# Performance work log

Measured on AMD Instinct MI355X. Metric: run time of the kernel, lower is better.

The kernel has to match this reference:

```python
import jax, jax.numpy as jnp
import numpy as np

N_NODES = 50000


def gcn_conv(x, W, b, src, dst, num_nodes):
    """PyG GCNConv: add self-loops, symmetric deg^{-1/2} normalization,
    linear transform, scatter-add aggregation, bias."""
    loop = jnp.arange(num_nodes, dtype=src.dtype)
    s = jnp.concatenate([src, loop])  # message sources
    d = jnp.concatenate([dst, loop])  # message destinations
    deg = jax.ops.segment_sum(jnp.ones_like(d, dtype=x.dtype), d, num_segments=num_nodes)
    dinv = jnp.where(deg > 0, jax.lax.rsqrt(deg), 0.0)
    norm = dinv[s] * dinv[d]                      # [E+N]
    h = x @ W                                      # [N, out]
    msg = h[s] * norm[:, None]                     # gather + scale  [E+N, out]
    out = jax.ops.segment_sum(msg, d, num_segments=num_nodes)  # scatter-add
    return out + b


def setup_inputs() -> dict:
    key = jax.random.key(0)
    ks = jax.random.split(key, 8)
    n, e = N_NODES, 1600000
    d_in, d_h, d_out = 128, 128, 64
    x = jax.random.normal(ks[0], (n, d_in), dtype=jnp.float32)
    edge_index = jax.random.randint(ks[1], (2, e), 0, n, dtype=jnp.int32)
    s = 1.0 / np.sqrt(d_in)
    W1 = jax.random.uniform(ks[2], (d_in, d_h), jnp.float32, -s, s)
    b1 = jnp.zeros((d_h,), jnp.float32)
    W2 = jax.random.uniform(ks[3], (d_h, d_h), jnp.float32, -s, s)
    b2 = jnp.zeros((d_h,), jnp.float32)
    W3 = jax.random.uniform(ks[4], (d_h, d_out), jnp.float32, -s, s)
    b3 = jnp.zeros((d_out,), jnp.float32)
    return {"x": x, "edge_index": edge_index, "W1": W1, "b1": b1,
            "W2": W2, "b2": b2, "W3": W3, "b3": b3}


def reference(x, edge_index, W1, b1, W2, b2, W3, b3):
    src, dst = edge_index[0], edge_index[1]
    n = x.shape[0]
    # Dropout in eval mode (identity); ReLU between GCN layers.
    h = jax.nn.relu(gcn_conv(x, W1, b1, src, dst, n))
    h = jax.nn.relu(gcn_conv(h, W2, b2, src, dst, n))
    out = gcn_conv(h, W3, b3, src, dst, n)
    return out
```

## Files before the change

kernel.cpp:

```cpp
#include <hip/hip_runtime.h>
#include <type_traits>


#define EPB  4096
#define DIRW 197

typedef __attribute__((ext_vector_type(8))) short bf16x8;
typedef __attribute__((ext_vector_type(4))) float f32x4;
typedef __attribute__((ext_vector_type(2))) float f32x2;

__device__ __forceinline__ unsigned short f2bf(float f) {
    unsigned int u = __float_as_uint(f);
    u += 0x7FFFu + ((u >> 16) & 1u);
    return (unsigned short)(u >> 16);
}
__device__ __forceinline__ float bflo(unsigned int u) { return __uint_as_float(u << 16); }
__device__ __forceinline__ float bfhi(unsigned int u) { return __uint_as_float(u & 0xFFFF0000u); }

__global__ __launch_bounds__(256) void bin_kernel(const int* __restrict__ src,
                                                  const int* __restrict__ dst,
                                                  unsigned int* __restrict__ pair_buf,
                                                  int* __restrict__ dir,
                                                  int E, int nbkt) {
    __shared__ unsigned int stage[EPB];
    __shared__ int hist[DIRW];
    __shared__ int sc[256];
    __shared__ int cur[DIRW];
    int tid = threadIdx.x;
    int blk = blockIdx.x;
    if (tid < DIRW) hist[tid] = 0;
    __syncthreads();

    int s_reg[16], d_reg[16];
#pragma unroll
    for (int j = 0; j < 16; ++j) {
        int gi = blk * EPB + j * 256 + tid;
        int s = 0, d = nbkt << 8;
        if (gi < E) { s = src[gi]; d = dst[gi]; }
        s_reg[j] = s; d_reg[j] = d;
        atomicAdd(&hist[d >> 8], 1);
    }
    __syncthreads();
    int h = (tid < DIRW) ? hist[tid] : 0;
    sc[tid] = h;
    __syncthreads();
#pragma unroll
    for (int off = 1; off < 256; off <<= 1) {
        int v = (tid >= off) ? sc[tid - off] : 0;
        __syncthreads();
        sc[tid] += v;
        __syncthreads();
    }
    if (tid < DIRW) {
        int st = sc[tid] - h;
        cur[tid] = st;
        dir[blk * DIRW + tid] = st;
    }
    __syncthreads();
#pragma unroll
    for (int j = 0; j < 16; ++j) {
        int b = d_reg[j] >> 8;
        int slot = atomicAdd(&cur[b], 1);
        stage[slot] = ((unsigned int)s_reg[j] << 8) | (unsigned int)(d_reg[j] & 255);
    }
    __syncthreads();
#pragma unroll
    for (int j = 0; j < 16; ++j) {
        int idx = j * 256 + tid;
        pair_buf[blk * EPB + idx] = stage[idx];
    }
}

__global__ __launch_bounds__(512) void csr_sizes_kernel(const unsigned int* __restrict__ pair_buf,
                                                        const int* __restrict__ dir,
                                                        int* __restrict__ bucket_pad,
                                                        int* __restrict__ node_cnt,
                                                        float* __restrict__ dinv,
                                                        int NB, int n) {
    __shared__ int dstart[400];
    __shared__ int dend[400];
    __shared__ int cnt[256];
    int tid = threadIdx.x;
    int b = blockIdx.x;
    for (int i = tid; i < NB; i += 512) {
        dstart[i] = dir[i * DIRW + b];
        dend[i]   = dir[i * DIRW + b + 1];
    }
    if (tid < 256) cnt[tid] = 0;
    __syncthreads();
    int wid = tid >> 6, lane = tid & 63;
    for (int seg = wid; seg < NB; seg += 8) {
        int s0 = dstart[seg], s1 = dend[seg];
        for (int k = s0 + lane; k < s1; k += 64) {
            unsigned int p = pair_buf[(size_t)seg * EPB + k];
            atomicAdd(&cnt[p & 255u], 1);
        }
    }
    __syncthreads();
    if (tid < 256) {
        node_cnt[b * 256 + tid] = cnt[tid];
        int d = b * 256 + tid;
        if (d < n) dinv[d] = rsqrtf((float)(cnt[tid] + 1));
    }
    if (tid < 64) {
        int m = max(max(cnt[4 * tid], cnt[4 * tid + 1]),
                    max(cnt[4 * tid + 2], cnt[4 * tid + 3]));
        int L = (m + 7) & ~7;
        int s = L;
#pragma unroll
        for (int off = 1; off < 64; off <<= 1) s += __shfl_xor(s, off);
        if (tid == 0) bucket_pad[b] = 4 * s;
    }
}

__global__ __launch_bounds__(256) void bucket_scan_kernel(const int* __restrict__ bucket_pad,
                                                          int* __restrict__ bucket_base,
                                                          int* __restrict__ row_ptr,
                                                          unsigned int* __restrict__ hb_pad_row,
                                                          int nbkt, int n) {
    __shared__ int sc[256];
    int tid = threadIdx.x;
    if (tid < 32) hb_pad_row[tid] = 0u;
    int h = (tid < nbkt) ? bucket_pad[tid] : 0;
    sc[tid] = h;
    __syncthreads();
#pragma unroll
    for (int off = 1; off < 256; off <<= 1) {
        int v = (tid >= off) ? sc[tid - off] : 0;
        __syncthreads();
        sc[tid] += v;
        __syncthreads();
    }
    if (tid <= nbkt) bucket_base[tid] = sc[tid] - h;
    if (tid == nbkt) row_ptr[n] = sc[tid] - h;
}

__global__ __launch_bounds__(512) void csr_place_kernel(const unsigned int* __restrict__ pair_buf,
                                                        const int* __restrict__ dir,
                                                        const int* __restrict__ bucket_base,
                                                        const int* __restrict__ node_cnt,
                                                        int* __restrict__ row_ptr,
                                                        int* __restrict__ csr_src,
                                                        int n, int NB) {
    __shared__ int dstart[400];
    __shared__ int dend[400];
    __shared__ int Lg[64];
    __shared__ int Lpre[64];
    __shared__ int nbase[256];
    __shared__ int cur[256];
    __shared__ int cend[256];
    int tid = threadIdx.x;
    int b = blockIdx.x;
    for (int i = tid; i < NB; i += 512) {
        dstart[i] = dir[i * DIRW + b];
        dend[i]   = dir[i * DIRW + b + 1];
    }
    __syncthreads();
    if (tid < 64) {
        int c0 = node_cnt[b * 256 + 4 * tid + 0];
        int c1 = node_cnt[b * 256 + 4 * tid + 1];
        int c2 = node_cnt[b * 256 + 4 * tid + 2];
        int c3 = node_cnt[b * 256 + 4 * tid + 3];
        int m = max(max(c0, c1), max(c2, c3));
        int L = (m + 7) & ~7;
        int x = L;
#pragma unroll
        for (int off = 1; off < 64; off <<= 1) {
            int y = __shfl_up(x, off);
            if (tid >= off) x += y;
        }
        Lg[tid] = L;
        Lpre[tid] = x - L;
    }
    __syncthreads();
    int base = bucket_base[b];
    if (tid < 256) {
        int g = tid >> 2;
        int nb = base + 4 * Lpre[g] + (tid & 3) * Lg[g];
        nbase[tid] = nb;
        cur[tid] = nb;
        cend[tid] = nb + Lg[g];
        int d = b * 256 + tid;
        if (d < n) row_ptr[d] = nb;
    }
    __syncthreads();
    int wid = tid >> 6, lane = tid & 63;
    for (int seg = wid; seg < NB; seg += 8) {
        int s0 = dstart[seg], s1 = dend[seg];
        for (int k = s0 + lane; k < s1; k += 64) {
            unsigned int p = pair_buf[(size_t)seg * EPB + k];
            int pos = atomicAdd(&cur[p & 255u], 1);
            csr_src[pos] = (int)(p >> 8);
        }
    }
    __syncthreads();
    if (tid < 256) {
        for (int pos = cur[tid]; pos < cend[tid]; ++pos) csr_src[pos] = n;
    }
}

__global__ __launch_bounds__(256) void wtrans_kernel(const float* __restrict__ W1,
                                                     const float* __restrict__ W2,
                                                     const float* __restrict__ W3,
                                                     unsigned short* __restrict__ Wt1,
                                                     unsigned short* __restrict__ Wt2,
                                                     unsigned short* __restrict__ Wt3) {
    int blk = blockIdx.x;
    const float* W; unsigned short* Wt; int N, e0;
    if (blk < 64)       { W = W1; Wt = Wt1; N = 128; e0 = blk * 256; }
    else if (blk < 128) { W = W2; Wt = Wt2; N = 128; e0 = (blk - 64) * 256; }
    else                { W = W3; Wt = Wt3; N = 64;  e0 = (blk - 128) * 256; }
    int e = e0 + threadIdx.x;
    int nn = e >> 7, k = e & 127;
    Wt[e] = f2bf(W[(size_t)k * N + nn]);
}

template <int NOUT, typename TA, bool FP8OUT>
__global__ __launch_bounds__(256) void gemm_bf16_kernel(const TA* __restrict__ X,
                                                        const unsigned short* __restrict__ Wt,
                                                        const float* __restrict__ dinv,
                                                        void* __restrict__ Hout,
                                                        int n_rows) {
    __shared__ short As[64][136];
    __shared__ short Bs[NOUT][136];
    int tid = threadIdx.x;
    int row0 = blockIdx.x * 64;

    {
        int r = tid >> 2;
        int c0 = (tid & 3) * 32;
        int grow = row0 + r;
        if constexpr (std::is_same<TA, float>::value) {
            const float* xp = X + (size_t)grow * 128 + c0;
#pragma unroll
            for (int j = 0; j < 8; ++j) {
                float4 v = (grow < n_rows) ? *(const float4*)(xp + j * 4)
                                           : make_float4(0.f, 0.f, 0.f, 0.f);
                ushort4 p = { f2bf(v.x), f2bf(v.y), f2bf(v.z), f2bf(v.w) };
                *(ushort4*)&As[r][c0 + j * 4] = p;
            }
        } else {
            const unsigned short* xp = X + (size_t)grow * 128 + c0;
#pragma unroll
            for (int j = 0; j < 8; ++j) {
                uint2 v = (grow < n_rows) ? *(const uint2*)(xp + j * 4)
                                          : make_uint2(0u, 0u);
                *(uint2*)&As[r][c0 + j * 4] = v;
            }
        }
    }
    {
        constexpr int TPR = 256 / NOUT;
        constexpr int CH  = 128 / TPR;
        int nrow = tid / TPR;
        int seg  = tid % TPR;
        const unsigned short* wp = Wt + (size_t)nrow * 128 + seg * CH;
#pragma unroll
        for (int j = 0; j < CH / 8; ++j)
            *(uint4*)&Bs[nrow][seg * CH + j * 8] = *(const uint4*)(wp + j * 8);
    }
    __syncthreads();

    int w = tid >> 6, l = tid & 63, lr = l & 15, lg = l >> 4;
    constexpr int NF = NOUT / 16;
    f32x4 acc[NF];
#pragma unroll
    for (int i = 0; i < NF; ++i) acc[i] = (f32x4){0.f, 0.f, 0.f, 0.f};
    int arow = w * 16 + lr;

#pragma unroll
    for (int kc = 0; kc < 128; kc += 32) {
        bf16x8 a;
        ((long long*)&a)[0] = *(const long long*)&As[arow][kc + lg * 4];
        ((long long*)&a)[1] = *(const long long*)&As[arow][kc + 16 + lg * 4];
#pragma unroll
        for (int nf = 0; nf < NF; ++nf) {
            bf16x8 b;
            ((long long*)&b)[0] = *(const long long*)&Bs[nf * 16 + lr][kc + lg * 4];
            ((long long*)&b)[1] = *(const long long*)&Bs[nf * 16 + lr][kc + 16 + lg * 4];
            acc[nf] = __builtin_amdgcn_mfma_f32_16x16x32_bf16(a, b, acc[nf], 0, 0, 0);
        }
    }
    int grow_base = row0 + w * 16 + lg * 4;
    float dv[4];
#pragma unroll
    for (int r = 0; r < 4; ++r)
        dv[r] = (grow_base + r < n_rows) ? dinv[grow_base + r] : 0.f;
#pragma unroll
    for (int nf = 0; nf < NF; ++nf) {
#pragma unroll
        for (int r = 0; r < 4; ++r) {
            int gr = grow_base + r;
            if (gr < n_rows) {
                float val = acc[nf][r] * dv[r];
                if constexpr (FP8OUT) {
                    unsigned int pk = __builtin_amdgcn_cvt_pk_fp8_f32(val, val, 0, false);
                    ((unsigned char*)Hout)[(size_t)gr * NOUT + nf * 16 + lr] =
                        (unsigned char)(pk & 0xFFu);
                } else {
                    ((unsigned short*)Hout)[(size_t)gr * NOUT + nf * 16 + lr] = f2bf(val);
                }
            }
        }
    }
}

template <bool RELU>
__global__ __launch_bounds__(256) void agg128_kernel(const unsigned char* __restrict__ H,
                                                     const int* __restrict__ csr_src,
                                                     const int* __restrict__ row_ptr,
                                                     const float* __restrict__ dinv,
                                                     const float* __restrict__ bias,
                                                     unsigned short* __restrict__ out, int n) {
    int g = blockIdx.x * 4 + threadIdx.y;
    int node0 = g * 4;
    if (node0 >= n) return;
    int lane = threadIdx.x;
    int sub = lane >> 4, l16 = lane & 15;
    int node = node0 + sub;
    int base = row_ptr[node0];
    int L = (row_ptr[node0 + 4] - base) >> 2;
    int e0 = base + sub * L;
    const uint2* H2 = (const uint2*)H;
    float acc[8] = {0.f, 0.f, 0.f, 0.f, 0.f, 0.f, 0.f, 0.f};
    for (int k = 0; k < L; k += 8) {
        int idx[8];
#pragma unroll
        for (int j = 0; j < 8; ++j) idx[j] = csr_src[e0 + k + j];
        uint2 v[8];
#pragma unroll
        for (int j = 0; j < 8; ++j) v[j] = H2[(size_t)idx[j] * 16 + l16];
#pragma unroll
        for (int j = 0; j < 8; ++j) {
            f32x2 a0 = __builtin_amdgcn_cvt_pk_f32_fp8((int)v[j].x, false);
            f32x2 a1 = __builtin_amdgcn_cvt_pk_f32_fp8((int)v[j].x, true);
            f32x2 a2 = __builtin_amdgcn_cvt_pk_f32_fp8((int)v[j].y, false);
            f32x2 a3 = __builtin_amdgcn_cvt_pk_f32_fp8((int)v[j].y, true);
            acc[0] += a0.x; acc[1] += a0.y; acc[2] += a1.x; acc[3] += a1.y;
            acc[4] += a2.x; acc[5] += a2.y; acc[6] += a3.x; acc[7] += a3.y;
        }
    }
    uint2 vn = H2[(size_t)node * 16 + l16];
    {
        f32x2 a0 = __builtin_amdgcn_cvt_pk_f32_fp8((int)vn.x, false);
        f32x2 a1 = __builtin_amdgcn_cvt_pk_f32_fp8((int)vn.x, true);
        f32x2 a2 = __builtin_amdgcn_cvt_pk_f32_fp8((int)vn.y, false);
        f32x2 a3 = __builtin_amdgcn_cvt_pk_f32_fp8((int)vn.y, true);
        acc[0] += a0.x; acc[1] += a0.y; acc[2] += a1.x; acc[3] += a1.y;
        acc[4] += a2.x; acc[5] += a2.y; acc[6] += a3.x; acc[7] += a3.y;
    }
    float dn = dinv[node];
    const float4* b4 = (const float4*)(bias + l16 * 8);
    float4 bb0 = b4[0], bb1 = b4[1];
    float r0 = fmaf(acc[0], dn, bb0.x), r1 = fmaf(acc[1], dn, bb0.y);
    float r2 = fmaf(acc[2], dn, bb0.z), r3 = fmaf(acc[3], dn, bb0.w);
    float r4 = fmaf(acc[4], dn, bb1.x), r5 = fmaf(acc[5], dn, bb1.y);
    float r6 = fmaf(acc[6], dn, bb1.z), r7 = fmaf(acc[7], dn, bb1.w);
    if (RELU) {
        r0 = fmaxf(r0, 0.f); r1 = fmaxf(r1, 0.f); r2 = fmaxf(r2, 0.f); r3 = fmaxf(r3, 0.f);
        r4 = fmaxf(r4, 0.f); r5 = fmaxf(r5, 0.f); r6 = fmaxf(r6, 0.f); r7 = fmaxf(r7, 0.f);
    }
    uint4 pk;
    pk.x = ((unsigned int)f2bf(r1) << 16) | (unsigned int)f2bf(r0);
    pk.y = ((unsigned int)f2bf(r3) << 16) | (unsigned int)f2bf(r2);
    pk.z = ((unsigned int)f2bf(r5) << 16) | (unsigned int)f2bf(r4);
    pk.w = ((unsigned int)f2bf(r7) << 16) | (unsigned int)f2bf(r6);
    ((uint4*)out)[(size_t)node * 16 + l16] = pk;
}

__global__ __launch_bounds__(256) void agg64_kernel(const unsigned short* __restrict__ H,
                                                    const int* __restrict__ csr_src,
                                                    const int* __restrict__ row_ptr,
                                                    const float* __restrict__ dinv,
                                                    const float* __restrict__ bias,
                                                    float* __restrict__ out, int n) {
    int g = blockIdx.x * 4 + threadIdx.y;
    int node0 = g * 4;
    if (node0 >= n) return;
    int lane = threadIdx.x;
    int sub = lane >> 4, l16 = lane & 15;
    int node = node0 + sub;
    int base = row_ptr[node0];
    int L = (row_ptr[node0 + 4] - base) >> 2;
    int e0 = base + sub * L;
    const uint2* H2 = (const uint2*)H;
    float acc[4] = {0.f, 0.f, 0.f, 0.f};
    for (int k = 0; k < L; k += 8) {
        int idx[8];
#pragma unroll
        for (int j = 0; j < 8; ++j) idx[j] = csr_src[e0 + k + j];
        uint2 v[8];
#pragma unroll
        for (int j = 0; j < 8; ++j) v[j] = H2[(size_t)idx[j] * 16 + l16];
#pragma unroll
        for (int j = 0; j < 8; ++j) {
            acc[0] += bflo(v[j].x); acc[1] += bfhi(v[j].x);
            acc[2] += bflo(v[j].y); acc[3] += bfhi(v[j].y);
        }
    }
    uint2 vn = H2[(size_t)node * 16 + l16];
    acc[0] += bflo(vn.x); acc[1] += bfhi(vn.x);
    acc[2] += bflo(vn.y); acc[3] += bfhi(vn.y);
    float dn = dinv[node];
    float4 bb = *(const float4*)(bias + l16 * 4);
    float4 r;
    r.x = fmaf(acc[0], dn, bb.x);
    r.y = fmaf(acc[1], dn, bb.y);
    r.z = fmaf(acc[2], dn, bb.z);
    r.w = fmaf(acc[3], dn, bb.w);
    *(float4*)(out + (size_t)node * 64 + l16 * 4) = r;
}

extern "C" void kernel_launch(void* const* d_in, const int* in_sizes, int n_in,
                              void* d_out, int out_size, void* d_ws, size_t ws_size,
                              hipStream_t stream) {
    const float* x  = (const float*)d_in[0];
    const int*   ei = (const int*)d_in[1];
    const float* W1 = (const float*)d_in[2];
    const float* b1 = (const float*)d_in[3];
    const float* W2 = (const float*)d_in[4];
    const float* b2 = (const float*)d_in[5];
    const float* W3 = (const float*)d_in[6];
    const float* b3 = (const float*)d_in[7];

    const int n = in_sizes[0] / 128;
    const int E = in_sizes[1] / 2;
    const int* src = ei;
    const int* dst = ei + E;
    const int nbkt = (n + 255) >> 8;
    const int NB = (E + EPB - 1) / EPB;

    char* ws = (char*)d_ws;
    size_t off = 0;
    auto alloc = [&](size_t bytes) {
        void* p = ws + off;
        off = (off + bytes + 511) & ~(size_t)511;
        return p;
    };
    int*   bucket_pad  = (int*)alloc(256 * 4);
    int*   bucket_base = (int*)alloc(512 * 4);
    int*   row_ptr     = (int*)alloc((size_t)(n + 1) * 4);
    float* dinv        = (float*)alloc((size_t)n * 4);
    int*   node_cnt    = (int*)alloc((size_t)nbkt * 256 * 4);
    int*   csr_src     = (int*)alloc((size_t)4000000 * 4);
    unsigned short* Wt1 = (unsigned short*)alloc(128 * 128 * 2);
    unsigned short* Wt2 = (unsigned short*)alloc(128 * 128 * 2);
    unsigned short* Wt3 = (unsigned short*)alloc(64 * 128 * 2);
    unsigned char* Hb  = (unsigned char*)alloc((size_t)(n + 1) * 128);
    unsigned short* Bb = (unsigned short*)alloc((size_t)n * 128 * 2);
    unsigned int* pair_buf = (unsigned int*)Bb;
    int*          dir      = (int*)((char*)Bb + (size_t)NB * EPB * 4);
    (void)ws_size;

    bin_kernel<<<NB, 256, 0, stream>>>(src, dst, pair_buf, dir, E, nbkt);
    csr_sizes_kernel<<<nbkt, 512, 0, stream>>>(pair_buf, dir, bucket_pad, node_cnt, dinv, NB, n);
    bucket_scan_kernel<<<1, 256, 0, stream>>>(bucket_pad, bucket_base, row_ptr,
                                              (unsigned int*)(Hb + (size_t)n * 128), nbkt, n);
    csr_place_kernel<<<nbkt, 512, 0, stream>>>(pair_buf, dir, bucket_base, node_cnt,
                                               row_ptr, csr_src, n, NB);
    wtrans_kernel<<<160, 256, 0, stream>>>(W1, W2, W3, Wt1, Wt2, Wt3);

    dim3 aggBlock(64, 4);
    int aggGrid = (n / 4 + 3) / 4;
    int gemmGrid = (n + 63) / 64;

    gemm_bf16_kernel<128, float, true><<<gemmGrid, 256, 0, stream>>>(x, Wt1, dinv, Hb, n);
    agg128_kernel<true><<<aggGrid, aggBlock, 0, stream>>>(Hb, csr_src, row_ptr, dinv, b1, Bb, n);
    gemm_bf16_kernel<128, unsigned short, true><<<gemmGrid, 256, 0, stream>>>(Bb, Wt2, dinv, Hb, n);
    agg128_kernel<true><<<aggGrid, aggBlock, 0, stream>>>(Hb, csr_src, row_ptr, dinv, b2, Bb, n);
    gemm_bf16_kernel<64, unsigned short, false><<<gemmGrid, 256, 0, stream>>>(Bb, Wt3, dinv, Hb, n);
    agg64_kernel<<<aggGrid, aggBlock, 0, stream>>>((unsigned short*)Hb, csr_src, row_ptr,
                                                   dinv, b3, (float*)d_out, n);
}
```

Baseline: 198.7 us.

## Split CSR rows into low/high source halves and fuse weight transpose into scan

Each destination's CSR row is now laid out as two padded sub-segments, with neighbors whose source index is in the lower half of the node range placed first and those in the upper half after. The intent is better locality in the gather during aggregation, since neighbors from the same half of the feature table are read together. Because of the separate rounding to multiples of 8, each row can carry up to one extra block of padding, and the low/high counts are packed into one int with 16 bits each. Separately, the weight-transpose kernel is merged into the single-block bucket scan launch to save one kernel launch.

```diff
diff --git a/kernel.cpp b/kernel.cpp
--- a/kernel.cpp
+++ b/kernel.cpp
@@ -79,33 +79,39 @@
                                                         int NB, int n) {
     __shared__ int dstart[400];
     __shared__ int dend[400];
-    __shared__ int cnt[256];
+    __shared__ int cnt_lo[256];
+    __shared__ int cnt_hi[256];
     int tid = threadIdx.x;
     int b = blockIdx.x;
+    int half = n >> 1;
     for (int i = tid; i < NB; i += 512) {
         dstart[i] = dir[i * DIRW + b];
         dend[i]   = dir[i * DIRW + b + 1];
     }
-    if (tid < 256) cnt[tid] = 0;
+    if (tid < 256) { cnt_lo[tid] = 0; cnt_hi[tid] = 0; }
     __syncthreads();
     int wid = tid >> 6, lane = tid & 63;
     for (int seg = wid; seg < NB; seg += 8) {
         int s0 = dstart[seg], s1 = dend[seg];
         for (int k = s0 + lane; k < s1; k += 64) {
             unsigned int p = pair_buf[(size_t)seg * EPB + k];
-            atomicAdd(&cnt[p & 255u], 1);
+            int s = (int)(p >> 8);
+            if (s < half) atomicAdd(&cnt_lo[p & 255u], 1);
+            else          atomicAdd(&cnt_hi[p & 255u], 1);
         }
     }
     __syncthreads();
     if (tid < 256) {
-        node_cnt[b * 256 + tid] = cnt[tid];
+        node_cnt[b * 256 + tid] = cnt_lo[tid] | (cnt_hi[tid] << 16);
         int d = b * 256 + tid;
-        if (d < n) dinv[d] = rsqrtf((float)(cnt[tid] + 1));
+        if (d < n) dinv[d] = rsqrtf((float)(cnt_lo[tid] + cnt_hi[tid] + 1));
     }
     if (tid < 64) {
-        int m = max(max(cnt[4 * tid], cnt[4 * tid + 1]),
-                    max(cnt[4 * tid + 2], cnt[4 * tid + 3]));
-        int L = (m + 7) & ~7;
+        int mlo = max(max(cnt_lo[4 * tid], cnt_lo[4 * tid + 1]),
+                      max(cnt_lo[4 * tid + 2], cnt_lo[4 * tid + 3]));
+        int mhi = max(max(cnt_hi[4 * tid], cnt_hi[4 * tid + 1]),
+                      max(cnt_hi[4 * tid + 2], cnt_hi[4 * tid + 3]));
+        int L = ((mlo + 7) & ~7) + ((mhi + 7) & ~7);
         int s = L;
 #pragma unroll
         for (int off = 1; off < 64; off <<= 1) s += __shfl_xor(s, off);
@@ -113,26 +119,43 @@
     }
 }
 
-__global__ __launch_bounds__(256) void bucket_scan_kernel(const int* __restrict__ bucket_pad,
+__global__ __launch_bounds__(256) void scan_wtrans_kernel(const int* __restrict__ bucket_pad,
                                                           int* __restrict__ bucket_base,
                                                           int* __restrict__ row_ptr,
                                                           unsigned int* __restrict__ hb_pad_row,
-                                                          int nbkt, int n) {
-    __shared__ int sc[256];
-    int tid = threadIdx.x;
-    if (tid < 32) hb_pad_row[tid] = 0u;
-    int h = (tid < nbkt) ? bucket_pad[tid] : 0;
-    sc[tid] = h;
-    __syncthreads();
-#pragma unroll
-    for (int off = 1; off < 256; off <<= 1) {
-        int v = (tid >= off) ? sc[tid - off] : 0;
+                                                          int nbkt, int n,
+                                                          const float* __restrict__ W1,
+                                                          const float* __restrict__ W2,
+                                                          const float* __restrict__ W3,
+                                                          unsigned short* __restrict__ Wt1,
+                                                          unsigned short* __restrict__ Wt2,
+                                                          unsigned short* __restrict__ Wt3) {
+    if (blockIdx.x == 0) {
+        __shared__ int sc[256];
+        int tid = threadIdx.x;
+        if (tid < 32) hb_pad_row[tid] = 0u;
+        int h = (tid < nbkt) ? bucket_pad[tid] : 0;
+        sc[tid] = h;
         __syncthreads();
-        sc[tid] += v;
-        __syncthreads();
-    }
-    if (tid <= nbkt) bucket_base[tid] = sc[tid] - h;
-    if (tid == nbkt) row_ptr[n] = sc[tid] - h;
+#pragma unroll
+        for (int off = 1; off < 256; off <<= 1) {
+            int v = (tid >= off) ? sc[tid - off] : 0;
+            __syncthreads();
+            sc[tid] += v;
+            __syncthreads();
+        }
+        if (tid <= nbkt) bucket_base[tid] = sc[tid] - h;
+        if (tid == nbkt) row_ptr[n] = sc[tid] - h;
+    } else {
+        int blk = blockIdx.x - 1;
+        const float* W; unsigned short* Wt; int N, e0;
+        if (blk < 64)       { W = W1; Wt = Wt1; N = 128; e0 = blk * 256; }
+        else if (blk < 128) { W = W2; Wt = Wt2; N = 128; e0 = (blk - 64) * 256; }
+        else                { W = W3; Wt = Wt3; N = 64;  e0 = (blk - 128) * 256; }
+        int e = e0 + threadIdx.x;
+        int nn = e >> 7, k = e & 127;
+        Wt[e] = f2bf(W[(size_t)k * N + nn]);
+    }
 }
 
 __global__ __launch_bounds__(512) void csr_place_kernel(const unsigned int* __restrict__ pair_buf,
@@ -144,13 +167,15 @@
                                                         int n, int NB) {
     __shared__ int dstart[400];
     __shared__ int dend[400];
+    __shared__ int Llo[64];
     __shared__ int Lg[64];
     __shared__ int Lpre[64];
     __shared__ int nbase[256];
-    __shared__ int cur[256];
-    __shared__ int cend[256];
+    __shared__ int cur_lo[256];
+    __shared__ int cur_hi[256];
     int tid = threadIdx.x;
     int b = blockIdx.x;
+    int half = n >> 1;
     for (int i = tid; i < NB; i += 512) {
         dstart[i] = dir[i * DIRW + b];
         dend[i]   = dir[i * DIRW + b + 1];
@@ -161,14 +186,17 @@
         int c1 = node_cnt[b * 256 + 4 * tid + 1];
         int c2 = node_cnt[b * 256 + 4 * tid + 2];
         int c3 = node_cnt[b * 256 + 4 * tid + 3];
-        int m = max(max(c0, c1), max(c2, c3));
-        int L = (m + 7) & ~7;
+        int mlo = max(max(c0 & 0xFFFF, c1 & 0xFFFF), max(c2 & 0xFFFF, c3 & 0xFFFF));
+        int mhi = max(max(c0 >> 16, c1 >> 16), max(c2 >> 16, c3 >> 16));
+        int llo = (mlo + 7) & ~7;
+        int L = llo + ((mhi + 7) & ~7);
         int x = L;
 #pragma unroll
         for (int off = 1; off < 64; off <<= 1) {
             int y = __shfl_up(x, off);
             if (tid >= off) x += y;
         }
+        Llo[tid] = llo;
         Lg[tid] = L;
         Lpre[tid] = x - L;
     }
@@ -178,8 +206,8 @@
         int g = tid >> 2;
         int nb = base + 4 * Lpre[g] + (tid & 3) * Lg[g];
         nbase[tid] = nb;
-        cur[tid] = nb;
-        cend[tid] = nb + Lg[g];
+        cur_lo[tid] = nb;
+        cur_hi[tid] = nb + Llo[g];
         int d = b * 256 + tid;
         if (d < n) row_ptr[d] = nb;
     }
@@ -189,30 +217,20 @@
         int s0 = dstart[seg], s1 = dend[seg];
         for (int k = s0 + lane; k < s1; k += 64) {
             unsigned int p = pair_buf[(size_t)seg * EPB + k];
-            int pos = atomicAdd(&cur[p & 255u], 1);
-            csr_src[pos] = (int)(p >> 8);
+            int s = (int)(p >> 8);
+            int pos = (s < half) ? atomicAdd(&cur_lo[p & 255u], 1)
+                                 : atomicAdd(&cur_hi[p & 255u], 1);
+            csr_src[pos] = s;
         }
     }
     __syncthreads();
     if (tid < 256) {
-        for (int pos = cur[tid]; pos < cend[tid]; ++pos) csr_src[pos] = n;
-    }
-}
-
-__global__ __launch_bounds__(256) void wtrans_kernel(const float* __restrict__ W1,
-                                                     const float* __restrict__ W2,
-                                                     const float* __restrict__ W3,
-                                                     unsigned short* __restrict__ Wt1,
-                                                     unsigned short* __restrict__ Wt2,
-                                                     unsigned short* __restrict__ Wt3) {
-    int blk = blockIdx.x;
-    const float* W; unsigned short* Wt; int N, e0;
-    if (blk < 64)       { W = W1; Wt = Wt1; N = 128; e0 = blk * 256; }
-    else if (blk < 128) { W = W2; Wt = Wt2; N = 128; e0 = (blk - 64) * 256; }
-    else                { W = W3; Wt = Wt3; N = 64;  e0 = (blk - 128) * 256; }
-    int e = e0 + threadIdx.x;
-    int nn = e >> 7, k = e & 127;
-    Wt[e] = f2bf(W[(size_t)k * N + nn]);
+        int g = tid >> 2;
+        int lo_end = nbase[tid] + Llo[g];
+        int hi_end = nbase[tid] + Lg[g];
+        for (int pos = cur_lo[tid]; pos < lo_end; ++pos) csr_src[pos] = n;
+        for (int pos = cur_hi[tid]; pos < hi_end; ++pos) csr_src[pos] = n;
+    }
 }
 
 template <int NOUT, typename TA, bool FP8OUT>
@@ -454,11 +472,11 @@
 
     bin_kernel<<<NB, 256, 0, stream>>>(src, dst, pair_buf, dir, E, nbkt);
     csr_sizes_kernel<<<nbkt, 512, 0, stream>>>(pair_buf, dir, bucket_pad, node_cnt, dinv, NB, n);
-    bucket_scan_kernel<<<1, 256, 0, stream>>>(bucket_pad, bucket_base, row_ptr,
-                                              (unsigned int*)(Hb + (size_t)n * 128), nbkt, n);
+    scan_wtrans_kernel<<<161, 256, 0, stream>>>(bucket_pad, bucket_base, row_ptr,
+                                                (unsigned int*)(Hb + (size_t)n * 128), nbkt, n,
+                                                W1, W2, W3, Wt1, Wt2, Wt3);
     csr_place_kernel<<<nbkt, 512, 0, stream>>>(pair_buf, dir, bucket_base, node_cnt,
                                                row_ptr, csr_src, n, NB);
-    wtrans_kernel<<<160, 256, 0, stream>>>(W1, W2, W3, Wt1, Wt2, Wt3);
 
     dim3 aggBlock(64, 4);
     int aggGrid = (n / 4 + 3) / 4;
```

Measured after the change: 208.5 us. 1.05x slower.

## Store CSR source indices as 16-bit and fold scan/wtrans kernels into neighbors

Applied to the files above, without the earlier changes.

CSR source indices are now stored as unsigned short and read eight at a time with a single 16-byte vector load in the aggregation kernels. This halves index traffic across the three gather passes. The weight-transpose work is folded into the binning kernel as extra blocks, and the bucket prefix scan is recomputed redundantly inside each csr_place block, removing two kernel launches. The 16-bit indices only hold while the node count plus the padding index stays below 65536, which holds for the 50000-node inputs but not for larger graphs.

```diff
diff --git a/kernel.cpp b/kernel.cpp
--- a/kernel.cpp
+++ b/kernel.cpp
@@ -17,17 +17,36 @@
 __device__ __forceinline__ float bflo(unsigned int u) { return __uint_as_float(u << 16); }
 __device__ __forceinline__ float bfhi(unsigned int u) { return __uint_as_float(u & 0xFFFF0000u); }
 
-__global__ __launch_bounds__(256) void bin_kernel(const int* __restrict__ src,
-                                                  const int* __restrict__ dst,
-                                                  unsigned int* __restrict__ pair_buf,
-                                                  int* __restrict__ dir,
-                                                  int E, int nbkt) {
+__global__ __launch_bounds__(256) void bin_wtrans_kernel(const int* __restrict__ src,
+                                                         const int* __restrict__ dst,
+                                                         unsigned int* __restrict__ pair_buf,
+                                                         int* __restrict__ dir,
+                                                         int E, int nbkt, int NB,
+                                                         const float* __restrict__ W1,
+                                                         const float* __restrict__ W2,
+                                                         const float* __restrict__ W3,
+                                                         unsigned short* __restrict__ Wt1,
+                                                         unsigned short* __restrict__ Wt2,
+                                                         unsigned short* __restrict__ Wt3,
+                                                         unsigned int* __restrict__ hb_pad_row) {
+    int blk = blockIdx.x;
+    if (blk >= NB) {
+        int wb = blk - NB;
+        const float* W; unsigned short* Wt; int N, e0;
+        if (wb < 64)       { W = W1; Wt = Wt1; N = 128; e0 = wb * 256; }
+        else if (wb < 128) { W = W2; Wt = Wt2; N = 128; e0 = (wb - 64) * 256; }
+        else               { W = W3; Wt = Wt3; N = 64;  e0 = (wb - 128) * 256; }
+        int e = e0 + threadIdx.x;
+        int nn = e >> 7, k = e & 127;
+        Wt[e] = f2bf(W[(size_t)k * N + nn]);
+        if (wb == 0 && threadIdx.x < 32) hb_pad_row[threadIdx.x] = 0u;
+        return;
+    }
     __shared__ unsigned int stage[EPB];
     __shared__ int hist[DIRW];
     __shared__ int sc[256];
     __shared__ int cur[DIRW];
     int tid = threadIdx.x;
-    int blk = blockIdx.x;
     if (tid < DIRW) hist[tid] = 0;
     __syncthreads();
 
@@ -113,37 +132,16 @@
     }
 }
 
-__global__ __launch_bounds__(256) void bucket_scan_kernel(const int* __restrict__ bucket_pad,
-                                                          int* __restrict__ bucket_base,
-                                                          int* __restrict__ row_ptr,
-                                                          unsigned int* __restrict__ hb_pad_row,
-                                                          int nbkt, int n) {
-    __shared__ int sc[256];
-    int tid = threadIdx.x;
-    if (tid < 32) hb_pad_row[tid] = 0u;
-    int h = (tid < nbkt) ? bucket_pad[tid] : 0;
-    sc[tid] = h;
-    __syncthreads();
-#pragma unroll
-    for (int off = 1; off < 256; off <<= 1) {
-        int v = (tid >= off) ? sc[tid - off] : 0;
-        __syncthreads();
-        sc[tid] += v;
-        __syncthreads();
-    }
-    if (tid <= nbkt) bucket_base[tid] = sc[tid] - h;
-    if (tid == nbkt) row_ptr[n] = sc[tid] - h;
-}
-
 __global__ __launch_bounds__(512) void csr_place_kernel(const unsigned int* __restrict__ pair_buf,
                                                         const int* __restrict__ dir,
-                                                        const int* __restrict__ bucket_base,
+                                                        const int* __restrict__ bucket_pad,
                                                         const int* __restrict__ node_cnt,
                                                         int* __restrict__ row_ptr,
-                                                        int* __restrict__ csr_src,
-                                                        int n, int NB) {
+                                                        unsigned short* __restrict__ csr_src,
+                                                        int n, int NB, int nbkt) {
     __shared__ int dstart[400];
     __shared__ int dend[400];
+    __shared__ int psc[256];
     __shared__ int Lg[64];
     __shared__ int Lpre[64];
     __shared__ int nbase[256];
@@ -155,7 +153,18 @@
         dstart[i] = dir[i * DIRW + b];
         dend[i]   = dir[i * DIRW + b + 1];
     }
-    __syncthreads();
+    if (tid < 256) psc[tid] = (tid < nbkt) ? bucket_pad[tid] : 0;
+    __syncthreads();
+#pragma unroll
+    for (int off = 1; off < 256; off <<= 1) {
+        int v = 0;
+        if (tid < 256 && tid >= off) v = psc[tid - off];
+        __syncthreads();
+        if (tid < 256) psc[tid] += v;
+        __syncthreads();
+    }
+    int base = (b > 0) ? psc[b - 1] : 0;
+    if (b == nbkt - 1 && tid == 0) row_ptr[n] = psc[nbkt - 1];
     if (tid < 64) {
         int c0 = node_cnt[b * 256 + 4 * tid + 0];
         int c1 = node_cnt[b * 256 + 4 * tid + 1];
@@ -173,7 +182,6 @@
         Lpre[tid] = x - L;
     }
     __syncthreads();
-    int base = bucket_base[b];
     if (tid < 256) {
         int g = tid >> 2;
         int nb = base + 4 * Lpre[g] + (tid & 3) * Lg[g];
@@ -190,29 +198,14 @@
         for (int k = s0 + lane; k < s1; k += 64) {
             unsigned int p = pair_buf[(size_t)seg * EPB + k];
             int pos = atomicAdd(&cur[p & 255u], 1);
-            csr_src[pos] = (int)(p >> 8);
+            csr_src[pos] = (unsigned short)(p >> 8);
         }
     }
     __syncthreads();
     if (tid < 256) {
-        for (int pos = cur[tid]; pos < cend[tid]; ++pos) csr_src[pos] = n;
-    }
-}
-
-__global__ __launch_bounds__(256) void wtrans_kernel(const float* __restrict__ W1,
-                                                     const float* __restrict__ W2,
-                                                     const float* __restrict__ W3,
-                                                     unsigned short* __restrict__ Wt1,
-                                                     unsigned short* __restrict__ Wt2,
-                                                     unsigned short* __restrict__ Wt3) {
-    int blk = blockIdx.x;
-    const float* W; unsigned short* Wt; int N, e0;
-    if (blk < 64)       { W = W1; Wt = Wt1; N = 128; e0 = blk * 256; }
-    else if (blk < 128) { W = W2; Wt = Wt2; N = 128; e0 = (blk - 64) * 256; }
-    else                { W = W3; Wt = Wt3; N = 64;  e0 = (blk - 128) * 256; }
-    int e = e0 + threadIdx.x;
-    int nn = e >> 7, k = e & 127;
-    Wt[e] = f2bf(W[(size_t)k * N + nn]);
+        for (int pos = cur[tid]; pos < cend[tid]; ++pos)
+            csr_src[pos] = (unsigned short)n;
+    }
 }
 
 template <int NOUT, typename TA, bool FP8OUT>
@@ -307,7 +300,7 @@
 
 template <bool RELU>
 __global__ __launch_bounds__(256) void agg128_kernel(const unsigned char* __restrict__ H,
-                                                     const int* __restrict__ csr_src,
+                                                     const unsigned short* __restrict__ csr_src,
                                                      const int* __restrict__ row_ptr,
                                                      const float* __restrict__ dinv,
                                                      const float* __restrict__ bias,
@@ -324,9 +317,11 @@
     const uint2* H2 = (const uint2*)H;
     float acc[8] = {0.f, 0.f, 0.f, 0.f, 0.f, 0.f, 0.f, 0.f};
     for (int k = 0; k < L; k += 8) {
-        int idx[8];
-#pragma unroll
-        for (int j = 0; j < 8; ++j) idx[j] = csr_src[e0 + k + j];
+        uint4 iv = *(const uint4*)(csr_src + e0 + k);
+        int idx[8] = { (int)(iv.x & 0xFFFFu), (int)(iv.x >> 16),
+                       (int)(iv.y & 0xFFFFu), (int)(iv.y >> 16),
+                       (int)(iv.z & 0xFFFFu), (int)(iv.z >> 16),
+                       (int)(iv.w & 0xFFFFu), (int)(iv.w >> 16) };
         uint2 v[8];
 #pragma unroll
         for (int j = 0; j < 8; ++j) v[j] = H2[(size_t)idx[j] * 16 + l16];
@@ -369,7 +364,7 @@
 }
 
 __global__ __launch_bounds__(256) void agg64_kernel(const unsigned short* __restrict__ H,
-                                                    const int* __restrict__ csr_src,
+                                                    const unsigned short* __restrict__ csr_src,
                                                     const int* __restrict__ row_ptr,
                                                     const float* __restrict__ dinv,
                                                     const float* __restrict__ bias,
@@ -386,9 +381,11 @@
     const uint2* H2 = (const uint2*)H;
     float acc[4] = {0.f, 0.f, 0.f, 0.f};
     for (int k = 0; k < L; k += 8) {
-        int idx[8];
-#pragma unroll
-        for (int j = 0; j < 8; ++j) idx[j] = csr_src[e0 + k + j];
+        uint4 iv = *(const uint4*)(csr_src + e0 + k);
+        int idx[8] = { (int)(iv.x & 0xFFFFu), (int)(iv.x >> 16),
+                       (int)(iv.y & 0xFFFFu), (int)(iv.y >> 16),
+                       (int)(iv.z & 0xFFFFu), (int)(iv.z >> 16),
+                       (int)(iv.w & 0xFFFFu), (int)(iv.w >> 16) };
         uint2 v[8];
 #pragma unroll
         for (int j = 0; j < 8; ++j) v[j] = H2[(size_t)idx[j] * 16 + l16];
@@ -438,11 +435,10 @@
         return p;
     };
     int*   bucket_pad  = (int*)alloc(256 * 4);
-    int*   bucket_base = (int*)alloc(512 * 4);
     int*   row_ptr     = (int*)alloc((size_t)(n + 1) * 4);
     float* dinv        = (float*)alloc((size_t)n * 4);
     int*   node_cnt    = (int*)alloc((size_t)nbkt * 256 * 4);
-    int*   csr_src     = (int*)alloc((size_t)4000000 * 4);
+    unsigned short* csr_src = (unsigned short*)alloc((size_t)4000000 * 2);
     unsigned short* Wt1 = (unsigned short*)alloc(128 * 128 * 2);
     unsigned short* Wt2 = (unsigned short*)alloc(128 * 128 * 2);
     unsigned short* Wt3 = (unsigned short*)alloc(64 * 128 * 2);
@@ -452,13 +448,12 @@
     int*          dir      = (int*)((char*)Bb + (size_t)NB * EPB * 4);
     (void)ws_size;
 
-    bin_kernel<<<NB, 256, 0, stream>>>(src, dst, pair_buf, dir, E, nbkt);
+    bin_wtrans_kernel<<<NB + 160, 256, 0, stream>>>(src, dst, pair_buf, dir, E, nbkt, NB,
+                                                    W1, W2, W3, Wt1, Wt2, Wt3,
+                                                    (unsigned int*)(Hb + (size_t)n * 128));
     csr_sizes_kernel<<<nbkt, 512, 0, stream>>>(pair_buf, dir, bucket_pad, node_cnt, dinv, NB, n);
-    bucket_scan_kernel<<<1, 256, 0, stream>>>(bucket_pad, bucket_base, row_ptr,
-                                              (unsigned int*)(Hb + (size_t)n * 128), nbkt, n);
-    csr_place_kernel<<<nbkt, 512, 0, stream>>>(pair_buf, dir, bucket_base, node_cnt,
-                                               row_ptr, csr_src, n, NB);
-    wtrans_kernel<<<160, 256, 0, stream>>>(W1, W2, W3, Wt1, Wt2, Wt3);
+    csr_place_kernel<<<nbkt, 512, 0, stream>>>(pair_buf, dir, bucket_pad, node_cnt,
+                                               row_ptr, csr_src, n, NB, nbkt);
 
     dim3 aggBlock(64, 4);
     int aggGrid = (n / 4 + 3) / 4;
```

Result: faster. 189.1 us, median of 2 (-4.8%).
